# Kernel tuning notes

Hardware: AMD Instinct MI355X
Metric: run time of the kernel (lower is better)

## Reference

```python
import math
import jax, jax.numpy as jnp
import numpy as np

HIDDEN = 256
FREQ = 256          # frequency_embedding_size
MASK_RATIO = 0.75
B, L, PD = 16, 4096, 512  # batch, num_patches, patch_dim = 2*16*16


def setup_inputs() -> dict:
    key = jax.random.key(0)
    ks = jax.random.split(key, 12)
    patches = jax.random.normal(ks[0], (B, L, PD), jnp.float32)
    # sorted segment ids -> contiguous segments per row (bincount/cumsum structure)
    sample_ids = jnp.sort(jax.random.randint(ks[1], (B, L), 0, 8), axis=1).astype(jnp.int32)
    effective_lens = (jax.random.randint(ks[2], (B,), 0, 2048) + L // 2).astype(jnp.int32)
    noise = jax.random.uniform(ks[3], (B, L), dtype=jnp.float32)
    fs = jax.random.uniform(ks[4], (B,), dtype=jnp.float32) * 1000.0
    W = jax.random.normal(ks[5], (HIDDEN, PD), jnp.float32) * 0.02   # projection.weight
    b = jnp.zeros((HIDDEN,), jnp.float32)                            # projection.bias
    pos = jax.random.normal(ks[6], (L, HIDDEN), jnp.float32) * 0.02  # position_embeddings
    w1 = jax.random.normal(ks[7], (HIDDEN, FREQ), jnp.float32) * 0.02
    b1 = jnp.zeros((HIDDEN,), jnp.float32)
    w2 = jax.random.normal(ks[8], (HIDDEN, HIDDEN), jnp.float32) * 0.02
    b2 = jnp.zeros((HIDDEN,), jnp.float32)
    return {"patches": patches, "sample_ids": sample_ids,
            "effective_lens": effective_lens, "noise": noise, "fs": fs,
            "W": W, "b": b, "pos": pos, "w1": w1, "b1": b1, "w2": w2, "b2": b2}


def timestep_embedding(t, dim=FREQ, max_period=10000.0):
    half = dim // 2
    freqs = jnp.exp(-math.log(max_period) * jnp.arange(half, dtype=jnp.float32) / half)
    args = t[:, None] * freqs[None, :]
    return jnp.concatenate([jnp.cos(args), jnp.sin(args)], axis=-1)  # [B, FREQ]


def reference(patches, sample_ids, effective_lens, noise, fs,
              W, b, pos, w1, b1, w2, b2):
    Bb, Ll, _ = patches.shape
    # patch projection + position embeddings
    emb = jnp.einsum('blp,hp->blh', patches, W) + b + pos[None]  # [B, L, H]
    # timestep (fs) embedding: Linear -> SiLU -> Linear
    t_freq = timestep_embedding(fs)
    fs_emb = jax.nn.silu(t_freq @ w1.T + b1) @ w2.T + b2  # [B, H]

    j = jnp.arange(Ll)[None, :]
    valid = j < effective_lens[:, None]                       # key-pad mask
    prev = jnp.concatenate([jnp.full((Bb, 1), -1, sample_ids.dtype),
                            sample_ids[:, :-1]], axis=1)
    seg_start = valid & (sample_ids != prev)                  # cls-token slots
    fs_tok = valid & jnp.concatenate([jnp.zeros((Bb, 1), bool),
                                      seg_start[:, :-1]], axis=1)  # fs-token slots
    # prefix (cls+fs) tokens get noise 0 -> always kept; padding -> inf
    nz = jnp.where(seg_start | fs_tok, 0.0, noise)
    nz = jnp.where(valid, nz, jnp.inf)

    num_samples = seg_start.sum(axis=1).astype(jnp.int32)
    keep_f = (effective_lens - 2 * num_samples).astype(jnp.float32) * (1.0 - MASK_RATIO)
    len_keep = 2 * num_samples + jnp.trunc(keep_f).astype(jnp.int32)

    ids_shuffle = jnp.argsort(nz, axis=1)                     # [B, L]
    keep = j < len_keep[:, None]
    # partial re-sort: sort first len_keep kept indices per row
    prefix_sorted = jnp.sort(jnp.where(keep, ids_shuffle, Ll), axis=1)
    ids_shuffle = jnp.where(keep, prefix_sorted, ids_shuffle)
    ids_restore = jnp.argsort(ids_shuffle, axis=1)

    gathered = jnp.take_along_axis(emb, ids_shuffle[..., None], axis=1)
    # fs conditioning added to kept tokens; padded (to L, masked) beyond len_keep
    seq_unmasked = jnp.where(keep[..., None], gathered + fs_emb[:, None, :], 0.0)

    mae_base = ((j >= len_keep[:, None]) & valid).astype(jnp.float32)
    mae_mask = jnp.take_along_axis(mae_base, ids_restore, axis=1)
    # fa2 path: no dense attn mask, just segment ids of kept tokens
    unmask_ids = jnp.where(keep,
                           jnp.take_along_axis(sample_ids, ids_shuffle, axis=1), -1)
    return seq_unmasked, mae_mask, ids_restore, unmask_ids
```

## Files before the change

kernel.cpp:

```cpp
#include <hip/hip_runtime.h>
#include <hip/hip_bf16.h>

#define BB 16
#define LL 4096
#define PDIM 512
#define HH 256
#define HALFD 128
#define MT 32

typedef short bf16x8 __attribute__((ext_vector_type(8)));
typedef float f32x4 __attribute__((ext_vector_type(4)));

__device__ __forceinline__ unsigned short f2bf(float f) {
  unsigned x = __float_as_uint(f);
  unsigned r = (x + 0x7FFFu + ((x >> 16) & 1u)) >> 16;
  return (unsigned short)r;
}

__device__ __forceinline__ unsigned long long make_key(
    const int* __restrict__ sid, const float* __restrict__ nrow, int eff, int j) {
  int s = sid[j];
  int sp = (j >= 1) ? sid[j - 1] : -1;
  int spp = (j >= 2) ? sid[j - 2] : -1;
  bool valid = j < eff;
  bool segs = valid && (s != sp);
  bool fst = valid && (j > 0) && (sp != spp);
  unsigned vb;
  if (!valid) vb = 0x7F800000u;
  else if (segs || fst) vb = 0u;
  else vb = __float_as_uint(nrow[j]);
  return (((unsigned long long)vb) << 32) | (unsigned)j;
}

__global__ __launch_bounds__(256) void prep_kernel(const float* __restrict__ W,
                                                   unsigned short* __restrict__ Wbf,
                                                   int* __restrict__ rank_ws) {
  int idx = blockIdx.x * 256 + threadIdx.x;
  Wbf[idx] = f2bf(W[idx]);
  if (idx < BB * LL) rank_ws[idx] = 0;
}

__global__ __launch_bounds__(256) void fsemb_kernel(
    const float* __restrict__ fs, const float* __restrict__ w1,
    const float* __restrict__ b1, const float* __restrict__ w2,
    const float* __restrict__ b2, float* __restrict__ fs_emb) {
  int b = blockIdx.x, h = threadIdx.x;
  __shared__ float tf[HH];
  __shared__ float hid[HH];
  float fv = fs[b];
  int i = h & (HALFD - 1);
  float freq = expf(-9.210340371976184f * (float)i / 128.0f);
  float arg = fv * freq;
  tf[h] = (h < HALFD) ? cosf(arg) : sinf(arg);
  __syncthreads();
  float acc = b1[h];
  const float* wr = w1 + (size_t)h * HH;
  for (int k = 0; k < HH; k += 4) {
    float4 w4 = *reinterpret_cast<const float4*>(&wr[k]);
    acc += tf[k] * w4.x + tf[k + 1] * w4.y + tf[k + 2] * w4.z + tf[k + 3] * w4.w;
  }
  hid[h] = acc / (1.0f + expf(-acc));
  __syncthreads();
  float acc2 = b2[h];
  const float* wr2 = w2 + (size_t)h * HH;
  for (int k = 0; k < HH; k += 4) {
    float4 w4 = *reinterpret_cast<const float4*>(&wr2[k]);
    acc2 += hid[k] * w4.x + hid[k + 1] * w4.y + hid[k + 2] * w4.z + hid[k + 3] * w4.w;
  }
  fs_emb[b * HH + h] = acc2;
}

__global__ __launch_bounds__(1024) void rank_kernel(
    const int* __restrict__ sample_ids, const int* __restrict__ eff_lens,
    const float* __restrict__ noise, int* __restrict__ rank_ws) {
  const int ks = blockIdx.x, eq = blockIdx.y, b = blockIdx.z, tid = threadIdx.x;
  __shared__ __align__(16) unsigned long long sk[1024];
  const int eff = eff_lens[b];
  const int* sid = sample_ids + (size_t)b * LL;
  const float* nrow = noise + (size_t)b * LL;

  sk[tid] = make_key(sid, nrow, eff, ks * 1024 + tid);
  __syncthreads();

  const int e = eq * 1024 + tid;
  const unsigned long long mykey = make_key(sid, nrow, eff, e);
  int cnt = 0;
#pragma unroll 4
  for (int k = 0; k < 1024; k += 2) {
    ulonglong2 kk = *reinterpret_cast<const ulonglong2*>(&sk[k]);
    cnt += (kk.x < mykey) ? 1 : 0;
    cnt += (kk.y < mykey) ? 1 : 0;
  }
  atomicAdd(&rank_ws[b * LL + e], cnt);
}

__global__ __launch_bounds__(1024) void finalize_kernel(
    const int* __restrict__ sample_ids, const int* __restrict__ eff_lens,
    const int* __restrict__ rank_ws, float* __restrict__ out_mae,
    float* __restrict__ out_restore, float* __restrict__ out_unmask,
    int* __restrict__ keep_idx, int* __restrict__ lk_arr) {
  const int b = blockIdx.x, tid = threadIdx.x;
  __shared__ int sc[2][1024];
  const int eff = eff_lens[b];
  const int* sid = sample_ids + (size_t)b * LL;

  int local_ns = 0;
  for (int j = tid; j < LL; j += 1024) {
    int s = sid[j];
    int sp = (j >= 1) ? sid[j - 1] : -1;
    if (j < eff && s != sp) local_ns++;
  }
  sc[0][tid] = local_ns;
  __syncthreads();
  for (int off = 512; off > 0; off >>= 1) {
    if (tid < off) sc[0][tid] += sc[0][tid + off];
    __syncthreads();
  }
  const int ns = sc[0][0];
  const int lk = 2 * ns + ((eff - 2 * ns) >> 2);
  __syncthreads();

  const int base = tid * 4;
  int r4[4], c4[4], cnt = 0;
  for (int q = 0; q < 4; ++q) {
    r4[q] = rank_ws[b * LL + base + q];
    c4[q] = (r4[q] < lk) ? 1 : 0;
    cnt += c4[q];
  }
  int cur = 0;
  sc[0][tid] = cnt;
  __syncthreads();
  for (int off = 1; off < 1024; off <<= 1) {
    int v = sc[cur][tid];
    if (tid >= off) v += sc[cur][tid - off];
    sc[cur ^ 1][tid] = v;
    __syncthreads();
    cur ^= 1;
  }
  int run = sc[cur][tid] - cnt;

  float4 rst, mmk;
  float* rp = &rst.x; float* mp = &mmk.x;
  for (int q = 0; q < 4; ++q) {
    int j = base + q;
    int r;
    if (c4[q]) {
      r = run;
      keep_idx[b * LL + run] = j;
      out_unmask[(size_t)b * LL + run] = (float)sid[j];
      run++;
    } else {
      r = r4[q];
    }
    rp[q] = (float)r;
    mp[q] = (r >= lk && r < eff) ? 1.0f : 0.0f;
  }
  *reinterpret_cast<float4*>(out_restore + (size_t)b * LL + base) = rst;
  *reinterpret_cast<float4*>(out_mae + (size_t)b * LL + base) = mmk;

  for (int p = tid; p < LL; p += 1024)
    if (p >= lk) out_unmask[(size_t)b * LL + p] = -1.0f;
  if (tid == 0) lk_arr[b] = lk;
}

__global__ __launch_bounds__(256) void proj_kernel(
    const float* __restrict__ patches, const unsigned short* __restrict__ Wbf,
    const float* __restrict__ bias, const float* __restrict__ pos,
    const float* __restrict__ fs_emb, const int* __restrict__ keep_idx,
    const int* __restrict__ lk_arr, float* __restrict__ out0) {
  const int tile = blockIdx.x, b = blockIdx.y, tid = threadIdx.x;
  const int p0 = tile * MT;
  int lk = lk_arr[b];
  lk = lk < 0 ? 0 : (lk > LL ? LL : lk);
  float* outB = out0 + ((size_t)b * LL + p0) * HH;
  int nt = lk - p0;
  nt = nt > MT ? MT : nt;

  if (nt <= 0) {
    float4 z = make_float4(0.f, 0.f, 0.f, 0.f);
    float4* o4 = reinterpret_cast<float4*>(outB);
#pragma unroll
    for (int i = 0; i < MT * HH / 4 / 256; ++i)
      o4[i * 256 + tid] = z;
    return;
  }

  __shared__ __align__(16) unsigned short pA[MT * 520];
  __shared__ int idxs[MT];
  if (tid < MT) idxs[tid] = (tid < nt) ? (keep_idx[b * LL + p0 + tid] & (LL - 1)) : 0;
  __syncthreads();

  {
    const int r = tid >> 3, kc = (tid & 7) * 64;
    const float* prow = patches + ((size_t)b * LL + (size_t)idxs[r]) * PDIM + kc;
#pragma unroll
    for (int i = 0; i < 16; ++i) {
      float4 v = reinterpret_cast<const float4*>(prow)[i];
      ushort4 u = make_ushort4(f2bf(v.x), f2bf(v.y), f2bf(v.z), f2bf(v.w));
      *reinterpret_cast<ushort4*>(&pA[r * 520 + kc + i * 4]) = u;
    }
  }
  __syncthreads();

  const int lane = tid & 63, w = tid >> 6;
  const int li = lane & 15, q = lane >> 4;
  f32x4 zero4 = {0.f, 0.f, 0.f, 0.f};
  f32x4 acc[2][4];
#pragma unroll
  for (int m = 0; m < 2; ++m)
#pragma unroll
    for (int n = 0; n < 4; ++n) acc[m][n] = zero4;

#pragma unroll 2
  for (int k0 = 0; k0 < PDIM; k0 += 32) {
    bf16x8 a0 = *reinterpret_cast<const bf16x8*>(&pA[li * 520 + k0 + q * 8]);
    bf16x8 a1 = *reinterpret_cast<const bf16x8*>(&pA[(16 + li) * 520 + k0 + q * 8]);
#pragma unroll
    for (int n = 0; n < 4; ++n) {
      bf16x8 bf = *reinterpret_cast<const bf16x8*>(
          &Wbf[(size_t)(w * 64 + n * 16 + li) * PDIM + k0 + q * 8]);
      acc[0][n] = __builtin_amdgcn_mfma_f32_16x16x32_bf16(a0, bf, acc[0][n], 0, 0, 0);
      acc[1][n] = __builtin_amdgcn_mfma_f32_16x16x32_bf16(a1, bf, acc[1][n], 0, 0, 0);
    }
  }

#pragma unroll
  for (int m = 0; m < 2; ++m) {
#pragma unroll
    for (int n = 0; n < 4; ++n) {
      const int col = w * 64 + n * 16 + li;
      const float bv = bias[col] + fs_emb[b * HH + col];
#pragma unroll
      for (int rr = 0; rr < 4; ++rr) {
        const int trow = m * 16 + q * 4 + rr;
        float val = 0.f;
        if (p0 + trow < lk)
          val = acc[m][n][rr] + bv + pos[(size_t)idxs[trow] * HH + col];
        outB[(size_t)trow * HH + col] = val;
      }
    }
  }
}

extern "C" void kernel_launch(void* const* d_in, const int* in_sizes, int n_in,
                              void* d_out, int out_size, void* d_ws, size_t ws_size,
                              hipStream_t stream) {
  const float* patches = (const float*)d_in[0];
  const int* sample_ids = (const int*)d_in[1];
  const int* eff = (const int*)d_in[2];
  const float* noise = (const float*)d_in[3];
  const float* fs = (const float*)d_in[4];
  const float* W = (const float*)d_in[5];
  const float* bias = (const float*)d_in[6];
  const float* pos = (const float*)d_in[7];
  const float* w1 = (const float*)d_in[8];
  const float* b1 = (const float*)d_in[9];
  const float* w2 = (const float*)d_in[10];
  const float* b2 = (const float*)d_in[11];

  float* out0 = (float*)d_out;
  float* out_mae = out0 + (size_t)BB * LL * HH;
  float* out_restore = out_mae + (size_t)BB * LL;
  float* out_unmask = out_restore + (size_t)BB * LL;

  char* ws = (char*)d_ws;
  unsigned short* Wbf = (unsigned short*)ws;
  float* fs_emb = (float*)(ws + 262144);
  int* keep_idx = (int*)(ws + 278528);
  int* rank_ws = (int*)(ws + 540672);
  int* lk_arr = (int*)(ws + 802816);
  if (ws_size < 802880) return;

  prep_kernel<<<512, 256, 0, stream>>>(W, Wbf, rank_ws);
  fsemb_kernel<<<BB, 256, 0, stream>>>(fs, w1, b1, w2, b2, fs_emb);
  rank_kernel<<<dim3(4, 4, BB), 1024, 0, stream>>>(sample_ids, eff, noise, rank_ws);
  finalize_kernel<<<BB, 1024, 0, stream>>>(sample_ids, eff, rank_ws, out_mae,
                                           out_restore, out_unmask, keep_idx, lk_arr);
  proj_kernel<<<dim3(LL / MT, BB), 256, 0, stream>>>(patches, Wbf, bias, pos,
                                                     fs_emb, keep_idx, lk_arr, out0);
}
```

Measured before the change: 313.1 us.

## Merge prep and fs-embedding kernels, replace rank atomics with partial sums, warp-shuffle scans

Measured after the change: 311.4 us. Within noise of the previous version (-0.5%).

```diff
diff --git a/kernel.cpp b/kernel.cpp
--- a/kernel.cpp
+++ b/kernel.cpp
@@ -32,21 +32,19 @@
   return (((unsigned long long)vb) << 32) | (unsigned)j;
 }
 
-__global__ __launch_bounds__(256) void prep_kernel(const float* __restrict__ W,
-                                                   unsigned short* __restrict__ Wbf,
-                                                   int* __restrict__ rank_ws) {
-  int idx = blockIdx.x * 256 + threadIdx.x;
-  Wbf[idx] = f2bf(W[idx]);
-  if (idx < BB * LL) rank_ws[idx] = 0;
-}
-
-__global__ __launch_bounds__(256) void fsemb_kernel(
+__global__ __launch_bounds__(256) void prep_kernel(
+    const float* __restrict__ W, unsigned short* __restrict__ Wbf,
     const float* __restrict__ fs, const float* __restrict__ w1,
     const float* __restrict__ b1, const float* __restrict__ w2,
     const float* __restrict__ b2, float* __restrict__ fs_emb) {
-  int b = blockIdx.x, h = threadIdx.x;
   __shared__ float tf[HH];
   __shared__ float hid[HH];
+  if (blockIdx.x < 512) {
+    int idx = blockIdx.x * 256 + threadIdx.x;
+    Wbf[idx] = f2bf(W[idx]);
+    return;
+  }
+  const int b = blockIdx.x - 512, h = threadIdx.x;
   float fv = fs[b];
   int i = h & (HALFD - 1);
   float freq = expf(-9.210340371976184f * (float)i / 128.0f);
@@ -70,37 +68,44 @@
   fs_emb[b * HH + h] = acc2;
 }
 
-__global__ __launch_bounds__(1024) void rank_kernel(
+__global__ __launch_bounds__(512) void rank_kernel(
     const int* __restrict__ sample_ids, const int* __restrict__ eff_lens,
-    const float* __restrict__ noise, int* __restrict__ rank_ws) {
-  const int ks = blockIdx.x, eq = blockIdx.y, b = blockIdx.z, tid = threadIdx.x;
+    const float* __restrict__ noise, int* __restrict__ rank_part) {
+  const int oq = blockIdx.x, os = blockIdx.y, b = blockIdx.z, tid = threadIdx.x;
   __shared__ __align__(16) unsigned long long sk[1024];
   const int eff = eff_lens[b];
   const int* sid = sample_ids + (size_t)b * LL;
   const float* nrow = noise + (size_t)b * LL;
 
-  sk[tid] = make_key(sid, nrow, eff, ks * 1024 + tid);
-  __syncthreads();
-
-  const int e = eq * 1024 + tid;
-  const unsigned long long mykey = make_key(sid, nrow, eff, e);
-  int cnt = 0;
-#pragma unroll 4
+  sk[tid] = make_key(sid, nrow, eff, os * 1024 + tid);
+  sk[tid + 512] = make_key(sid, nrow, eff, os * 1024 + tid + 512);
+  const int e0 = oq * 1024 + tid * 2;
+  const unsigned long long k0 = make_key(sid, nrow, eff, e0);
+  const unsigned long long k1 = make_key(sid, nrow, eff, e0 + 1);
+  __syncthreads();
+
+  int c0 = 0, c1 = 0;
+#pragma unroll 8
   for (int k = 0; k < 1024; k += 2) {
     ulonglong2 kk = *reinterpret_cast<const ulonglong2*>(&sk[k]);
-    cnt += (kk.x < mykey) ? 1 : 0;
-    cnt += (kk.y < mykey) ? 1 : 0;
-  }
-  atomicAdd(&rank_ws[b * LL + e], cnt);
+    c0 += (kk.x < k0) ? 1 : 0;
+    c0 += (kk.y < k0) ? 1 : 0;
+    c1 += (kk.x < k1) ? 1 : 0;
+    c1 += (kk.y < k1) ? 1 : 0;
+  }
+  int2 res = make_int2(c0, c1);
+  *reinterpret_cast<int2*>(&rank_part[((size_t)os * BB + b) * LL + e0]) = res;
 }
 
 __global__ __launch_bounds__(1024) void finalize_kernel(
     const int* __restrict__ sample_ids, const int* __restrict__ eff_lens,
-    const int* __restrict__ rank_ws, float* __restrict__ out_mae,
+    const int* __restrict__ rank_part, float* __restrict__ out_mae,
     float* __restrict__ out_restore, float* __restrict__ out_unmask,
     int* __restrict__ keep_idx, int* __restrict__ lk_arr) {
   const int b = blockIdx.x, tid = threadIdx.x;
-  __shared__ int sc[2][1024];
+  const int wid = tid >> 6, lane = tid & 63;
+  __shared__ int wsum[16];
+  __shared__ int lksh;
   const int eff = eff_lens[b];
   const int* sid = sample_ids + (size_t)b * LL;
 
@@ -110,37 +115,56 @@
     int sp = (j >= 1) ? sid[j - 1] : -1;
     if (j < eff && s != sp) local_ns++;
   }
-  sc[0][tid] = local_ns;
-  __syncthreads();
-  for (int off = 512; off > 0; off >>= 1) {
-    if (tid < off) sc[0][tid] += sc[0][tid + off];
-    __syncthreads();
-  }
-  const int ns = sc[0][0];
-  const int lk = 2 * ns + ((eff - 2 * ns) >> 2);
-  __syncthreads();
+#pragma unroll
+  for (int off = 32; off > 0; off >>= 1) local_ns += __shfl_down(local_ns, off);
+  if (lane == 0) wsum[wid] = local_ns;
+  __syncthreads();
+  if (wid == 0) {
+    int v = (lane < 16) ? wsum[lane] : 0;
+#pragma unroll
+    for (int off = 32; off > 0; off >>= 1) v += __shfl_down(v, off);
+    if (lane == 0) {
+      int ns = v;
+      lksh = 2 * ns + ((eff - 2 * ns) >> 2);
+    }
+  }
+  __syncthreads();
+  const int lk = lksh;
 
   const int base = tid * 4;
-  int r4[4], c4[4], cnt = 0;
-  for (int q = 0; q < 4; ++q) {
-    r4[q] = rank_ws[b * LL + base + q];
-    c4[q] = (r4[q] < lk) ? 1 : 0;
-    cnt += c4[q];
-  }
-  int cur = 0;
-  sc[0][tid] = cnt;
-  __syncthreads();
-  for (int off = 1; off < 1024; off <<= 1) {
-    int v = sc[cur][tid];
-    if (tid >= off) v += sc[cur][tid - off];
-    sc[cur ^ 1][tid] = v;
-    __syncthreads();
-    cur ^= 1;
-  }
-  int run = sc[cur][tid] - cnt;
+  int4 p0 = *reinterpret_cast<const int4*>(&rank_part[((size_t)0 * BB + b) * LL + base]);
+  int4 p1 = *reinterpret_cast<const int4*>(&rank_part[((size_t)1 * BB + b) * LL + base]);
+  int4 p2 = *reinterpret_cast<const int4*>(&rank_part[((size_t)2 * BB + b) * LL + base]);
+  int4 p3 = *reinterpret_cast<const int4*>(&rank_part[((size_t)3 * BB + b) * LL + base]);
+  int r4[4] = {p0.x + p1.x + p2.x + p3.x, p0.y + p1.y + p2.y + p3.y,
+               p0.z + p1.z + p2.z + p3.z, p0.w + p1.w + p2.w + p3.w};
+  int c4[4], cnt = 0;
+#pragma unroll
+  for (int q = 0; q < 4; ++q) { c4[q] = (r4[q] < lk) ? 1 : 0; cnt += c4[q]; }
+
+  int incl = cnt;
+#pragma unroll
+  for (int off = 1; off < 64; off <<= 1) {
+    int v = __shfl_up(incl, off);
+    if (lane >= off) incl += v;
+  }
+  if (lane == 63) wsum[wid] = incl;
+  __syncthreads();
+  if (wid == 0) {
+    int s = (lane < 16) ? wsum[lane] : 0;
+#pragma unroll
+    for (int off = 1; off < 16; off <<= 1) {
+      int v = __shfl_up(s, off);
+      if (lane >= off) s += v;
+    }
+    if (lane < 16) wsum[lane] = s;
+  }
+  __syncthreads();
+  int run = ((wid > 0) ? wsum[wid - 1] : 0) + incl - cnt;
 
   float4 rst, mmk;
   float* rp = &rst.x; float* mp = &mmk.x;
+#pragma unroll
   for (int q = 0; q < 4; ++q) {
     int j = base + q;
     int r;
@@ -267,14 +291,13 @@
   unsigned short* Wbf = (unsigned short*)ws;
   float* fs_emb = (float*)(ws + 262144);
   int* keep_idx = (int*)(ws + 278528);
-  int* rank_ws = (int*)(ws + 540672);
-  int* lk_arr = (int*)(ws + 802816);
-  if (ws_size < 802880) return;
-
-  prep_kernel<<<512, 256, 0, stream>>>(W, Wbf, rank_ws);
-  fsemb_kernel<<<BB, 256, 0, stream>>>(fs, w1, b1, w2, b2, fs_emb);
-  rank_kernel<<<dim3(4, 4, BB), 1024, 0, stream>>>(sample_ids, eff, noise, rank_ws);
-  finalize_kernel<<<BB, 1024, 0, stream>>>(sample_ids, eff, rank_ws, out_mae,
+  int* rank_part = (int*)(ws + 540672);
+  int* lk_arr = (int*)(ws + 1589248);
+  if (ws_size < 1589312) return;
+
+  prep_kernel<<<528, 256, 0, stream>>>(W, Wbf, fs, w1, b1, w2, b2, fs_emb);
+  rank_kernel<<<dim3(4, 4, BB), 512, 0, stream>>>(sample_ids, eff, noise, rank_part);
+  finalize_kernel<<<BB, 1024, 0, stream>>>(sample_ids, eff, rank_part, out_mae,
                                            out_restore, out_unmask, keep_idx, lk_arr);
   proj_kernel<<<dim3(LL / MT, BB), 256, 0, stream>>>(patches, Wbf, bias, pos,
                                                      fs_emb, keep_idx, lk_arr, out0);
```
